# Performance work log

Measured on AMD Instinct MI355X. Metric: run time of the kernel, lower is better.

The kernel has to match this reference:

```python
import jax, jax.numpy as jnp
import numpy as np

N, E, IN, H, C, T = 50000, 800000, 128, 64, 64, 2
F1, FO1 = H, H // T   # conv1: per-tower in/out feats
F2, FO2 = H, C // T   # conv2
STD_EPS = 1e-5
BN_EPS = 1e-5


def setup_inputs() -> dict:
    key = jax.random.key(0)
    ks = jax.random.split(key, 12)
    rn = lambda k, s, sc=0.05: jax.random.normal(k, s, jnp.float32) * sc
    return {
        "x": jax.random.normal(ks[0], (N, IN), jnp.float32),
        "embed_W": rn(ks[1], (IN, H)),
        "embed_b": jnp.zeros((H,), jnp.float32),
        "pre_W1": rn(ks[2], (T, 2 * F1, F1)),
        "pre_b1": jnp.zeros((T, F1), jnp.float32),
        "post_W1": rn(ks[3], (T, 13 * F1, FO1)),
        "post_b1": jnp.zeros((T, FO1), jnp.float32),
        "lin_W1": rn(ks[4], (H, H)),
        "lin_b1": jnp.zeros((H,), jnp.float32),
        "bn_gamma": jnp.ones((H,), jnp.float32),
        "bn_beta": jnp.zeros((H,), jnp.float32),
        "pre_W2": rn(ks[5], (T, 2 * F2, F2)),
        "pre_b2": jnp.zeros((T, F2), jnp.float32),
        "post_W2": rn(ks[6], (T, 13 * F2, FO2)),
        "post_b2": jnp.zeros((T, FO2), jnp.float32),
        "lin_W2": rn(ks[7], (C, C)),
        "lin_b2": jnp.zeros((C,), jnp.float32),
        "src": jax.random.randint(ks[8], (E,), 0, N, jnp.int32),
        "dst": jax.random.randint(ks[9], (E,), 0, N, jnp.int32),
    }


def _pna_conv(h, src, dst, deg_raw, degc, avg_log, preW, preb, postW, postb, linW, linb):
    # h: [N, F] node feats; messages flow src -> dst, aggregated at dst.
    m = jnp.concatenate([h[dst], h[src]], axis=-1)            # [E, 2F]  (cat[x_i, x_j])
    m = jnp.einsum('ef,tfg->etg', m, preW) + preb[None]       # [E, T, F] per-tower pre-NN
    seg = lambda v: jax.ops.segment_sum(v, dst, num_segments=N)
    cnt = degc[:, None, None]                                 # clamped degree >= 1
    has = (deg_raw > 0)[:, None, None]
    mean = seg(m) / cnt                                       # [N, T, F]
    mean_sq = seg(m * m) / cnt
    mn = jnp.where(has, jax.ops.segment_min(m, dst, num_segments=N), 0.0)
    mx = jnp.where(has, jax.ops.segment_max(m, dst, num_segments=N), 0.0)
    std = jnp.sqrt(jax.nn.relu(mean_sq - mean * mean) + STD_EPS)
    agg = jnp.concatenate([mean, mn, mx, std], axis=-1)       # [N, T, 4F]
    ld = jnp.log(degc + 1.0)[:, None, None]
    out = jnp.concatenate([agg, agg * (ld / avg_log), agg * (avg_log / ld)], axis=-1)  # [N, T, 12F]
    F = h.shape[-1]
    out = jnp.concatenate([jnp.broadcast_to(h[:, None, :], (N, T, F)), out], axis=-1)  # [N, T, 13F]
    out = jnp.einsum('ntf,tfg->ntg', out, postW) + postb[None]  # [N, T, FO] per-tower post-NN
    return out.reshape(N, -1) @ linW + linb                    # final mixing Linear(out, out)


def reference(x, embed_W, embed_b, pre_W1, pre_b1, post_W1, post_b1, lin_W1, lin_b1,
              bn_gamma, bn_beta, pre_W2, pre_b2, post_W2, post_b2, lin_W2, lin_b2,
              src, dst):
    deg_raw = jax.ops.segment_sum(jnp.ones((E,), jnp.float32), dst, num_segments=N)
    degc = jnp.maximum(deg_raw, 1.0)
    avg_log = jnp.mean(jnp.log(deg_raw + 1.0))  # avg_deg['log'] from the graph's degrees
    h = x @ embed_W + embed_b
    h = _pna_conv(h, src, dst, deg_raw, degc, avg_log,
                  pre_W1, pre_b1, post_W1, post_b1, lin_W1, lin_b1)
    mu = jnp.mean(h, axis=0)
    var = jnp.mean((h - mu) ** 2, axis=0)
    h = bn_gamma * (h - mu) / jnp.sqrt(var + BN_EPS) + bn_beta
    h = jax.nn.relu(h)  # dropout is identity in eval mode
    return _pna_conv(h, src, dst, deg_raw, degc, avg_log,
                     pre_W2, pre_b2, post_W2, post_b2, lin_W2, lin_b2)
```

## Files before the change

kernel.cpp:

```cpp
#include <hip/hip_runtime.h>

#define N_NODES 50000
#define E_EDGES 800000
#define IN_F    128
#define H_F     64
#define STD_EPS 1e-5f
#define BN_EPS  1e-5f

#define HIST_BLK 3125
#define EMB_BLK  768
#define SCAN_BLK 49
#define TRANS_BLK 448

__global__ __launch_bounds__(256) void k_hist_embed(const int* __restrict__ dst,
                                                    int* __restrict__ deg,
                                                    const float* __restrict__ x,
                                                    const float* __restrict__ W,
                                                    const float* __restrict__ bias,
                                                    float* __restrict__ h) {
  __shared__ float sW[IN_F * 64];
  __shared__ float sx[IN_F * 36];
  if (blockIdx.x < HIST_BLK) {
    int e = blockIdx.x * 256 + threadIdx.x;
    atomicAdd(&deg[dst[e]], 1);
    return;
  }
  for (int i = threadIdx.x; i < IN_F * 64; i += 256) sW[i] = W[i];
  int f = threadIdx.x & 63, ng = threadIdx.x >> 6;
  float bj = bias[f];
  const int NGRP = (N_NODES + 31) / 32;
  for (int grp = blockIdx.x - HIST_BLK; grp < NGRP; grp += EMB_BLK) {
    int n0 = grp * 32;
    __syncthreads();
    for (int idx = threadIdx.x; idx < 32 * IN_F; idx += 256) {
      int nl = idx >> 7, k = idx & 127;
      int n = n0 + nl;
      sx[k * 36 + nl] = (n < N_NODES) ? x[(size_t)n * IN_F + k] : 0.f;
    }
    __syncthreads();
    float a[8] = {bj, bj, bj, bj, bj, bj, bj, bj};
    const float* xp = &sx[ng * 8];
#pragma unroll 4
    for (int k = 0; k < IN_F; k++) {
      float4 h0 = *(const float4*)&xp[k * 36];
      float4 h1 = *(const float4*)&xp[k * 36 + 4];
      float w = sW[k * 64 + f];
      a[0] = fmaf(h0.x, w, a[0]); a[1] = fmaf(h0.y, w, a[1]);
      a[2] = fmaf(h0.z, w, a[2]); a[3] = fmaf(h0.w, w, a[3]);
      a[4] = fmaf(h1.x, w, a[4]); a[5] = fmaf(h1.y, w, a[5]);
      a[6] = fmaf(h1.z, w, a[6]); a[7] = fmaf(h1.w, w, a[7]);
    }
#pragma unroll
    for (int j = 0; j < 8; j++) {
      int n = n0 + ng * 8 + j;
      if (n < N_NODES) h[(size_t)n * 64 + f] = a[j];
    }
  }
}

__global__ __launch_bounds__(256) void k_scanpart_trans(const int* __restrict__ deg,
                                                        int* __restrict__ partials,
                                                        float* __restrict__ scalars,
                                                        const float* __restrict__ pW1,
                                                        const float* __restrict__ pW2,
                                                        const float* __restrict__ lW1,
                                                        const float* __restrict__ lW2,
                                                        float* __restrict__ pWT,
                                                        float* __restrict__ lWT) {
  __shared__ int red[256];
  __shared__ float redf[256];
  if (blockIdx.x < SCAN_BLK) {
    int base = blockIdx.x * 1024;
    int s = 0; float ls = 0.f;
    for (int j = threadIdx.x; j < 1024; j += 256) {
      int i = base + j;
      if (i < N_NODES) { int d = deg[i]; s += d; ls += logf((float)d + 1.0f); }
    }
    red[threadIdx.x] = s; redf[threadIdx.x] = ls; __syncthreads();
    for (int st = 128; st > 0; st >>= 1) {
      if (threadIdx.x < st) {
        red[threadIdx.x] += red[threadIdx.x + st];
        redf[threadIdx.x] += redf[threadIdx.x + st];
      }
      __syncthreads();
    }
    if (threadIdx.x == 0) {
      partials[blockIdx.x] = red[0];
      atomicAdd(&scalars[0], redf[0]);
    }
    return;
  }
  int idx = (blockIdx.x - SCAN_BLK) * 256 + threadIdx.x;
  if (idx < 106496) {
    int layer = idx / 53248, r = idx % 53248;
    int t = r / 26624, r2 = r % 26624;
    int fb = r2 / 128, r3 = r2 % 128;
    int g = r3 / 4, j = r3 % 4;
    const float* srcp = layer ? pW2 : pW1;
    pWT[idx] = srcp[(size_t)t * 26624 + (fb * 4 + j) * 32 + g];
  } else if (idx < 114688) {
    int jj = idx - 106496;
    int layer = jj / 4096, r2 = jj % 4096;
    int c4 = r2 / 256, r3 = r2 % 256;
    int col = r3 / 4, j = r3 % 4;
    const float* srcl = layer ? lW2 : lW1;
    lWT[jj] = srcl[(c4 * 4 + j) * 64 + col];
  }
}

__global__ __launch_bounds__(256) void k_scan_final(const int* __restrict__ deg,
                                                    const int* __restrict__ partials,
                                                    int* __restrict__ row_ptr,
                                                    int* __restrict__ cursor,
                                                    float* __restrict__ scalars) {
  __shared__ int ts[256];
  __shared__ int sbase;
  if (threadIdx.x == 0) {
    int pre = 0;
    for (int b = 0; b < (int)blockIdx.x; b++) pre += partials[b];
    sbase = pre;
    if (blockIdx.x == 0) {
      scalars[1] = scalars[0] / (float)N_NODES;
      row_ptr[N_NODES] = E_EDGES;
    }
  }
  int base = blockIdx.x * 1024 + threadIdx.x * 4;
  int d[4]; int s = 0;
#pragma unroll
  for (int j = 0; j < 4; j++) {
    int i = base + j;
    d[j] = (i < N_NODES) ? deg[i] : 0;
    s += d[j];
  }
  ts[threadIdx.x] = s; __syncthreads();
  for (int off = 1; off < 256; off <<= 1) {
    int t = (threadIdx.x >= off) ? ts[threadIdx.x - off] : 0;
    __syncthreads();
    ts[threadIdx.x] += t;
    __syncthreads();
  }
  int excl = (threadIdx.x > 0) ? ts[threadIdx.x - 1] : 0;
  int run = sbase + excl;
#pragma unroll
  for (int j = 0; j < 4; j++) {
    int i = base + j;
    if (i < N_NODES) { row_ptr[i] = run; cursor[i] = run; run += d[j]; }
  }
}

__global__ __launch_bounds__(256) void k_scatter(const int* __restrict__ src,
                                                 const int* __restrict__ dst,
                                                 int* __restrict__ cursor,
                                                 int* __restrict__ csr_src) {
  int e = blockIdx.x * 256 + threadIdx.x;
  if (e < E_EDGES) {
    int d = dst[e];
    int p = atomicAdd(&cursor[d], 1);
    csr_src[p] = src[e];
  }
}

template <bool BN>
__global__ __launch_bounds__(256) void k_preab(const float* __restrict__ hin,
                                               const float* __restrict__ preW,
                                               const float* __restrict__ preb,
                                               const float* __restrict__ bnsum,
                                               const float* __restrict__ bnsumsq,
                                               const float* __restrict__ gamma,
                                               const float* __restrict__ beta,
                                               float* __restrict__ h2out,
                                               float* __restrict__ hA,
                                               float* __restrict__ hB) {
  __shared__ float sWp[64 * 128];
  __shared__ float sh[64 * 68];
  __shared__ float sbn[128];
  int t = blockIdx.x & 1;
  const float* Wsrc = preW + (size_t)t * 128 * 64;
  for (int i = threadIdx.x; i < 64 * 64; i += 256) {
    int k = i >> 6, f = i & 63;
    float wa = Wsrc[k * 64 + f];
    float wb = Wsrc[(64 + k) * 64 + f];
    *(float2*)&sWp[k * 128 + f * 2] = make_float2(wa, wb);
  }
  if (BN && threadIdx.x < 64) {
    int c = threadIdx.x;
    float mu = bnsum[c] * (1.f / N_NODES);
    float var = bnsumsq[c] * (1.f / N_NODES) - mu * mu;
    float sc = gamma[c] / sqrtf(var + BN_EPS);
    sbn[c] = sc;
    sbn[64 + c] = fmaf(-mu, sc, beta[c]);
  }
  int f = threadIdx.x & 63, ng = threadIdx.x >> 6;
  float pb = preb[t * 64 + f];
  int nblk2 = gridDim.x >> 1;
  const int NGRP = (N_NODES + 63) / 64;
  for (int grp = blockIdx.x >> 1; grp < NGRP; grp += nblk2) {
    int n0 = grp * 64;
    __syncthreads();
    for (int idx = threadIdx.x; idx < 64 * 64; idx += 256) {
      int nl = idx >> 6, k = idx & 63;
      int n = n0 + nl;
      float v = 0.f;
      if (n < N_NODES) {
        v = hin[(size_t)n * 64 + k];
        if (BN) {
          v = fmaxf(fmaf(v, sbn[k], sbn[64 + k]), 0.f);
          if (t == 0) h2out[(size_t)n * 64 + k] = v;
        }
      }
      sh[k * 68 + nl] = v;
    }
    __syncthreads();
    float a[16], b[16];
#pragma unroll
    for (int j = 0; j < 16; j++) { a[j] = pb; b[j] = 0.f; }
    const float* hp = &sh[ng * 16];
    const float* wp = &sWp[f * 2];
#pragma unroll 2
    for (int k = 0; k < 64; k++) {
      float4 h0 = *(const float4*)&hp[k * 68];
      float4 h1 = *(const float4*)&hp[k * 68 + 4];
      float4 h2 = *(const float4*)&hp[k * 68 + 8];
      float4 h3 = *(const float4*)&hp[k * 68 + 12];
      float2 w2 = *(const float2*)&wp[k * 128];
      a[0]  = fmaf(h0.x, w2.x, a[0]);  b[0]  = fmaf(h0.x, w2.y, b[0]);
      a[1]  = fmaf(h0.y, w2.x, a[1]);  b[1]  = fmaf(h0.y, w2.y, b[1]);
      a[2]  = fmaf(h0.z, w2.x, a[2]);  b[2]  = fmaf(h0.z, w2.y, b[2]);
      a[3]  = fmaf(h0.w, w2.x, a[3]);  b[3]  = fmaf(h0.w, w2.y, b[3]);
      a[4]  = fmaf(h1.x, w2.x, a[4]);  b[4]  = fmaf(h1.x, w2.y, b[4]);
      a[5]  = fmaf(h1.y, w2.x, a[5]);  b[5]  = fmaf(h1.y, w2.y, b[5]);
      a[6]  = fmaf(h1.z, w2.x, a[6]);  b[6]  = fmaf(h1.z, w2.y, b[6]);
      a[7]  = fmaf(h1.w, w2.x, a[7]);  b[7]  = fmaf(h1.w, w2.y, b[7]);
      a[8]  = fmaf(h2.x, w2.x, a[8]);  b[8]  = fmaf(h2.x, w2.y, b[8]);
      a[9]  = fmaf(h2.y, w2.x, a[9]);  b[9]  = fmaf(h2.y, w2.y, b[9]);
      a[10] = fmaf(h2.z, w2.x, a[10]); b[10] = fmaf(h2.z, w2.y, b[10]);
      a[11] = fmaf(h2.w, w2.x, a[11]); b[11] = fmaf(h2.w, w2.y, b[11]);
      a[12] = fmaf(h3.x, w2.x, a[12]); b[12] = fmaf(h3.x, w2.y, b[12]);
      a[13] = fmaf(h3.y, w2.x, a[13]); b[13] = fmaf(h3.y, w2.y, b[13]);
      a[14] = fmaf(h3.z, w2.x, a[14]); b[14] = fmaf(h3.z, w2.y, b[14]);
      a[15] = fmaf(h3.w, w2.x, a[15]); b[15] = fmaf(h3.w, w2.y, b[15]);
    }
    int tf = t * 64 + f;
#pragma unroll
    for (int j = 0; j < 16; j++) {
      int n = n0 + ng * 16 + j;
      if (n < N_NODES) {
        hA[(size_t)n * 128 + tf] = a[j];
        hB[(size_t)n * 128 + tf] = b[j];
      }
    }
  }
}

__global__ __launch_bounds__(256, 7) void k_conv(const float* __restrict__ hA,
                                                 const float* __restrict__ hB,
                                                 const float* __restrict__ hskip,
                                                 const int* __restrict__ row_ptr,
                                                 const int* __restrict__ csr_src,
                                                 const float* __restrict__ postWT,
                                                 const float* __restrict__ postb,
                                                 const float* __restrict__ linWT,
                                                 const float* __restrict__ linb,
                                                 const float* __restrict__ scalars,
                                                 float* __restrict__ out) {
  __shared__ float sm[2 * 5 * 8 * 64];
  __shared__ float sAB[16];
  int w = threadIdx.x >> 6, lane = threadIdx.x & 63;
  int n0 = blockIdx.x * 8;
  int t = lane >> 5, fb2 = (lane & 31) * 2;
  int off = t * 64 + fb2;
  float avg = scalars[1];

#pragma unroll 1
  for (int k = 0; k < 2; k++) {
    int nl = w * 2 + k;
    int n = n0 + nl;
    float2 a = *(const float2*)&hA[(size_t)n * 128 + off];
    int rp0 = __builtin_amdgcn_readfirstlane(row_ptr[n]);
    int rp1 = __builtin_amdgcn_readfirstlane(row_ptr[n + 1]);
    float sx0=0,sy0=0,qx0=0,qy0=0, sx1=0,sy1=0,qx1=0,qy1=0;
    float mnx0=INFINITY,mny0=INFINITY,mxx0=-INFINITY,mxy0=-INFINITY;
    float mnx1=INFINITY,mny1=INFINITY,mxx1=-INFINITY,mxy1=-INFINITY;
    int i = rp0;
    int end4 = rp0 + ((rp1 - rp0) & ~3);
    if (i < end4) {
      int s0 = csr_src[i], s1 = csr_src[i+1], s2 = csr_src[i+2], s3 = csr_src[i+3];
      while (true) {
        float2 v0 = *(const float2*)&hB[(size_t)s0 * 128 + off];
        float2 v1 = *(const float2*)&hB[(size_t)s1 * 128 + off];
        float2 v2 = *(const float2*)&hB[(size_t)s2 * 128 + off];
        float2 v3 = *(const float2*)&hB[(size_t)s3 * 128 + off];
        i += 4;
        bool more = (i < end4);
        if (more) { s0 = csr_src[i]; s1 = csr_src[i+1]; s2 = csr_src[i+2]; s3 = csr_src[i+3]; }
        float e0x = v0.x + a.x, e0y = v0.y + a.y;
        float e1x = v1.x + a.x, e1y = v1.y + a.y;
        float e2x = v2.x + a.x, e2y = v2.y + a.y;
        float e3x = v3.x + a.x, e3y = v3.y + a.y;
        sx0 += e0x; qx0 = fmaf(e0x,e0x,qx0); mnx0 = fminf(mnx0,e0x); mxx0 = fmaxf(mxx0,e0x);
        sy0 += e0y; qy0 = fmaf(e0y,e0y,qy0); mny0 = fminf(mny0,e0y); mxy0 = fmaxf(mxy0,e0y);
        sx1 += e1x; qx1 = fmaf(e1x,e1x,qx1); mnx1 = fminf(mnx1,e1x); mxx1 = fmaxf(mxx1,e1x);
        sy1 += e1y; qy1 = fmaf(e1y,e1y,qy1); mny1 = fminf(mny1,e1y); mxy1 = fmaxf(mxy1,e1y);
        sx0 += e2x; qx0 = fmaf(e2x,e2x,qx0); mnx0 = fminf(mnx0,e2x); mxx0 = fmaxf(mxx0,e2x);
        sy0 += e2y; qy0 = fmaf(e2y,e2y,qy0); mny0 = fminf(mny0,e2y); mxy0 = fmaxf(mxy0,e2y);
        sx1 += e3x; qx1 = fmaf(e3x,e3x,qx1); mnx1 = fminf(mnx1,e3x); mxx1 = fmaxf(mxx1,e3x);
        sy1 += e3y; qy1 = fmaf(e3y,e3y,qy1); mny1 = fminf(mny1,e3y); mxy1 = fmaxf(mxy1,e3y);
        if (!more) break;
      }
    }
    {
      int r = rp1 - i;
      if (r > 0) {
        int e1i = (r > 1) ? i + 1 : i;
        int e2i = (r > 2) ? i + 2 : i;
        int t0 = csr_src[i], t1 = csr_src[e1i], t2 = csr_src[e2i];
        float2 u0 = *(const float2*)&hB[(size_t)t0 * 128 + off];
        float2 u1 = *(const float2*)&hB[(size_t)t1 * 128 + off];
        float2 u2 = *(const float2*)&hB[(size_t)t2 * 128 + off];
        float ex = u0.x + a.x, ey = u0.y + a.y;
        sx0 += ex; qx0 = fmaf(ex,ex,qx0); mnx0 = fminf(mnx0,ex); mxx0 = fmaxf(mxx0,ex);
        sy0 += ey; qy0 = fmaf(ey,ey,qy0); mny0 = fminf(mny0,ey); mxy0 = fmaxf(mxy0,ey);
        if (r > 1) {
          ex = u1.x + a.x; ey = u1.y + a.y;
          sx1 += ex; qx1 = fmaf(ex,ex,qx1); mnx1 = fminf(mnx1,ex); mxx1 = fmaxf(mxx1,ex);
          sy1 += ey; qy1 = fmaf(ey,ey,qy1); mny1 = fminf(mny1,ey); mxy1 = fmaxf(mxy1,ey);
        }
        if (r > 2) {
          ex = u2.x + a.x; ey = u2.y + a.y;
          sx0 += ex; qx0 = fmaf(ex,ex,qx0); mnx0 = fminf(mnx0,ex); mxx0 = fmaxf(mxx0,ex);
          sy0 += ey; qy0 = fmaf(ey,ey,qy0); mny0 = fminf(mny0,ey); mxy0 = fmaxf(mxy0,ey);
        }
      }
    }
    int dg = rp1 - rp0;
    float cnt = (float)(dg > 0 ? dg : 1);
    float inv = 1.0f / cnt;
    float meanx = (sx0 + sx1) * inv, meany = (sy0 + sy1) * inv;
    float qx = qx0 + qx1, qy = qy0 + qy1;
    float sdx = sqrtf(fmaxf(qx * inv - meanx * meanx, 0.f) + STD_EPS);
    float sdy = sqrtf(fmaxf(qy * inv - meany * meany, 0.f) + STD_EPS);
    float mnx = fminf(mnx0, mnx1), mny = fminf(mny0, mny1);
    float mxx = fmaxf(mxx0, mxx1), mxy = fmaxf(mxy0, mxy1);
    if (dg == 0) { mnx = 0; mny = 0; mxx = 0; mxy = 0; }
    float ldv = logf(cnt + 1.f);
    float2 hsv = *(const float2*)&hskip[(size_t)n * 64 + fb2];
    float* bp = &sm[t * 2560 + nl * 64 + fb2];
    *(float2*)&bp[0]    = hsv;
    *(float2*)&bp[512]  = make_float2(meanx, meany);
    *(float2*)&bp[1024] = make_float2(mnx, mny);
    *(float2*)&bp[1536] = make_float2(mxx, mxy);
    *(float2*)&bp[2048] = make_float2(sdx, sdy);
    if (lane == 0) { sAB[nl] = ldv / avg; sAB[8 + nl] = avg / ldv; }
  }
  __syncthreads();

  float g1[8] = {0,0,0,0,0,0,0,0};
  float g2[8] = {0,0,0,0,0,0,0,0};
  float g3[8] = {0,0,0,0,0,0,0,0};
  {
    int g = lane & 31, hf0 = w * 16, fb0 = w * 4;
    const float4* pw4 = (const float4*)postWT + (size_t)t * 6656 + g;
    const float* vb = &sm[t * 2560 + hf0];
#pragma unroll
    for (int jj = 0; jj < 4; jj++) {
      float4 wv = pw4[(fb0 + jj) * 32];
#pragma unroll
      for (int nn = 0; nn < 8; nn++) {
        float4 v = *(const float4*)&vb[nn * 64 + jj * 4];
        g1[nn] = fmaf(v.w, wv.w, fmaf(v.z, wv.z, fmaf(v.y, wv.y, fmaf(v.x, wv.x, g1[nn]))));
      }
    }
#pragma unroll
    for (int fa = 0; fa < 4; fa++) {
      const float* vfa = &vb[(1 + fa) * 512];
#pragma unroll
      for (int jj = 0; jj < 4; jj++) {
        int fb = 16 + fa * 16 + fb0 + jj;
        float4 w1v = pw4[fb * 32];
        float4 w2v = pw4[(fb + 64) * 32];
        float4 w3v = pw4[(fb + 128) * 32];
#pragma unroll
        for (int nn = 0; nn < 8; nn++) {
          float4 v = *(const float4*)&vfa[nn * 64 + jj * 4];
          g1[nn] = fmaf(v.w, w1v.w, fmaf(v.z, w1v.z, fmaf(v.y, w1v.y, fmaf(v.x, w1v.x, g1[nn]))));
          g2[nn] = fmaf(v.w, w2v.w, fmaf(v.z, w2v.z, fmaf(v.y, w2v.y, fmaf(v.x, w2v.x, g2[nn]))));
          g3[nn] = fmaf(v.w, w3v.w, fmaf(v.z, w3v.z, fmaf(v.y, w3v.y, fmaf(v.x, w3v.x, g3[nn]))));
        }
      }
    }
  }
  float o8[8];
#pragma unroll
  for (int nn = 0; nn < 8; nn++)
    o8[nn] = fmaf(sAB[8 + nn], g3[nn], fmaf(sAB[nn], g2[nn], g1[nn]));
  __syncthreads();

  {
    int sw = (w + (lane >> 4)) & 3;
#pragma unroll
    for (int nn = 0; nn < 8; nn++)
      sm[((nn * 64 + lane) << 2) + sw] = o8[nn];
  }
  __syncthreads();

  {
#pragma unroll
    for (int r = 0; r < 2; r++) {
      int idx = r * 256 + (int)threadIdx.x;
      float4 p = *(const float4*)&sm[idx << 2];
      sm[2048 + idx] = p.x + p.y + p.z + p.w + postb[idx & 63];
    }
  }
  __syncthreads();

  {
    float acc0 = linb[lane], acc1 = acc0;
    const float4* lw4 = (const float4*)linWT + lane;
    const float* p0 = &sm[2048 + (w * 2) * 64];
    const float* p1 = p0 + 64;
#pragma unroll
    for (int c4 = 0; c4 < 16; c4++) {
      float4 lwv = lw4[c4 * 64];
      float4 pa = *(const float4*)&p0[c4 * 4];
      float4 pb2 = *(const float4*)&p1[c4 * 4];
      acc0 = fmaf(pa.w, lwv.w, fmaf(pa.z, lwv.z, fmaf(pa.y, lwv.y, fmaf(pa.x, lwv.x, acc0))));
      acc1 = fmaf(pb2.w, lwv.w, fmaf(pb2.z, lwv.z, fmaf(pb2.y, lwv.y, fmaf(pb2.x, lwv.x, acc1))));
    }
    size_t ob = (size_t)(n0 + w * 2) * 64 + lane;
    out[ob] = acc0;
    out[ob + 64] = acc1;
  }
}

__global__ __launch_bounds__(256) void k_bnstats(const float* __restrict__ y,
                                                 float* __restrict__ bnsum,
                                                 float* __restrict__ bnsumsq) {
  __shared__ float r1[256], r2[256];
  int c = threadIdx.x & 63, r = threadIdx.x >> 6;
  float s = 0, q = 0;
  for (int n = blockIdx.x * 4 + r; n < N_NODES; n += gridDim.x * 4) {
    float v = y[(size_t)n * 64 + c];
    s += v; q = fmaf(v, v, q);
  }
  r1[threadIdx.x] = s; r2[threadIdx.x] = q; __syncthreads();
  if (threadIdx.x < 64) {
    s = r1[threadIdx.x] + r1[threadIdx.x + 64] + r1[threadIdx.x + 128] + r1[threadIdx.x + 192];
    q = r2[threadIdx.x] + r2[threadIdx.x + 64] + r2[threadIdx.x + 128] + r2[threadIdx.x + 192];
    atomicAdd(&bnsum[threadIdx.x], s);
    atomicAdd(&bnsumsq[threadIdx.x], q);
  }
}

extern "C" void kernel_launch(void* const* d_in, const int* in_sizes, int n_in,
                              void* d_out, int out_size, void* d_ws, size_t ws_size,
                              hipStream_t stream) {
  const float* x      = (const float*)d_in[0];
  const float* embW   = (const float*)d_in[1];
  const float* embB   = (const float*)d_in[2];
  const float* preW1  = (const float*)d_in[3];
  const float* preb1  = (const float*)d_in[4];
  const float* postW1 = (const float*)d_in[5];
  const float* postb1 = (const float*)d_in[6];
  const float* linW1  = (const float*)d_in[7];
  const float* linb1  = (const float*)d_in[8];
  const float* gamma  = (const float*)d_in[9];
  const float* beta   = (const float*)d_in[10];
  const float* preW2  = (const float*)d_in[11];
  const float* preb2  = (const float*)d_in[12];
  const float* postW2 = (const float*)d_in[13];
  const float* postb2 = (const float*)d_in[14];
  const float* linW2  = (const float*)d_in[15];
  const float* linb2  = (const float*)d_in[16];
  const int*   src    = (const int*)d_in[17];
  const int*   dst    = (const int*)d_in[18];
  float* out = (float*)d_out;

  char* w = (char*)d_ws;
  size_t o = 0;
  int*   deg     = (int*)(w + o);   o += (size_t)N_NODES * 4;
  float* scalars = (float*)(w + o); o += 64;
  float* bnsum   = (float*)(w + o); o += 256;
  float* bnsumsq = (float*)(w + o); o += 256;
  size_t zero_len = o;
  o = (o + 255) & ~(size_t)255;
  int* partials = (int*)(w + o);  o += 256;
  int* row_ptr  = (int*)(w + o);  o += (size_t)(N_NODES + 1) * 4; o = (o + 255) & ~(size_t)255;
  int* cursor   = (int*)(w + o);  o += (size_t)N_NODES * 4;       o = (o + 255) & ~(size_t)255;
  int* csr      = (int*)(w + o);  o += (size_t)E_EDGES * 4;       o = (o + 255) & ~(size_t)255;
  float* postWT = (float*)(w + o); o += (size_t)2 * 53248 * 4;
  float* linWT  = (float*)(w + o); o += (size_t)2 * 4096 * 4;
  float* h1 = (float*)(w + o); o += (size_t)N_NODES * 64 * 4;
  float* y1 = (float*)(w + o); o += (size_t)N_NODES * 64 * 4;
  float* h2 = (float*)(w + o); o += (size_t)N_NODES * 64 * 4;
  float* hA = (float*)(w + o); o += (size_t)N_NODES * 128 * 4;
  float* hB = (float*)(w + o); o += (size_t)N_NODES * 128 * 4;

  hipMemsetAsync(w, 0, zero_len, stream);

  k_hist_embed<<<HIST_BLK + EMB_BLK, 256, 0, stream>>>(dst, deg, x, embW, embB, h1);
  k_scanpart_trans<<<SCAN_BLK + TRANS_BLK, 256, 0, stream>>>(
      deg, partials, scalars, postW1, postW2, linW1, linW2, postWT, linWT);
  k_scan_final<<<SCAN_BLK, 256, 0, stream>>>(deg, partials, row_ptr, cursor, scalars);
  k_scatter<<<(E_EDGES + 255) / 256, 256, 0, stream>>>(src, dst, cursor, csr);

  k_preab<false><<<768, 256, 0, stream>>>(h1, preW1, preb1, nullptr, nullptr,
                                          nullptr, nullptr, nullptr, hA, hB);
  k_conv<<<N_NODES / 8, 256, 0, stream>>>(hA, hB, h1, row_ptr, csr,
                                          postWT, postb1, linWT, linb1, scalars, y1);
  k_bnstats<<<256, 256, 0, stream>>>(y1, bnsum, bnsumsq);
  k_preab<true><<<768, 256, 0, stream>>>(y1, preW2, preb2, bnsum, bnsumsq,
                                         gamma, beta, h2, hA, hB);
  k_conv<<<N_NODES / 8, 256, 0, stream>>>(hA, hB, h2, row_ptr, csr,
                                          postWT + 53248, postb2, linWT + 4096,
                                          linb2, scalars, out);
}
```

Measured before the change: 540.5 us.

## Run per-tower post-NN GEMM on bf16x3 MFMA instead of FP32 FMAs

```diff
diff --git a/kernel.cpp b/kernel.cpp
--- a/kernel.cpp
+++ b/kernel.cpp
@@ -11,6 +11,23 @@
 #define EMB_BLK  768
 #define SCAN_BLK 49
 #define TRANS_BLK 448
+
+typedef __attribute__((ext_vector_type(8))) short bf16x8;
+typedef __attribute__((ext_vector_type(4))) float f32x4;
+
+__device__ __forceinline__ unsigned bf16_rne(float f) {
+  unsigned u = __float_as_uint(f);
+  return (u + 0x7fffu + ((u >> 16) & 1u)) >> 16;
+}
+__device__ __forceinline__ void bf16_split2(float x, float y, unsigned& hi, unsigned& lo) {
+  unsigned hx = bf16_rne(x), hy = bf16_rne(y);
+  float rx = x - __uint_as_float(hx << 16);
+  float ry = y - __uint_as_float(hy << 16);
+  hi = hx | (hy << 16);
+  lo = bf16_rne(rx) | (bf16_rne(ry) << 16);
+}
+
+#define MFMA(acc, a, b) acc = __builtin_amdgcn_mfma_f32_16x16x32_bf16(a, b, acc, 0, 0, 0)
 
 __global__ __launch_bounds__(256) void k_hist_embed(const int* __restrict__ dst,
                                                     int* __restrict__ deg,
@@ -65,7 +82,8 @@
                                                         const float* __restrict__ pW2,
                                                         const float* __restrict__ lW1,
                                                         const float* __restrict__ lW2,
-                                                        float* __restrict__ pWT,
+                                                        unsigned short* __restrict__ WBhi,
+                                                        unsigned short* __restrict__ WBlo,
                                                         float* __restrict__ lWT) {
   __shared__ int red[256];
   __shared__ float redf[256];
@@ -92,12 +110,15 @@
   }
   int idx = (blockIdx.x - SCAN_BLK) * 256 + threadIdx.x;
   if (idx < 106496) {
-    int layer = idx / 53248, r = idx % 53248;
-    int t = r / 26624, r2 = r % 26624;
-    int fb = r2 / 128, r3 = r2 % 128;
-    int g = r3 / 4, j = r3 % 4;
-    const float* srcp = layer ? pW2 : pW1;
-    pWT[idx] = srcp[(size_t)t * 26624 + (fb * 4 + j) * 32 + g];
+    int f = idx % 832;
+    int rest = idx / 832;
+    int col = rest & 31, tt = rest >> 5;
+    const float* srcp = (tt >= 2) ? pW2 : pW1;
+    float v = srcp[((size_t)(tt & 1) * 832 + f) * 32 + col];
+    unsigned hb = bf16_rne(v);
+    float rsd = v - __uint_as_float(hb << 16);
+    WBhi[idx] = (unsigned short)hb;
+    WBlo[idx] = (unsigned short)bf16_rne(rsd);
   } else if (idx < 114688) {
     int jj = idx - 106496;
     int layer = jj / 4096, r2 = jj % 4096;
@@ -252,18 +273,20 @@
   }
 }
 
-__global__ __launch_bounds__(256, 7) void k_conv(const float* __restrict__ hA,
+__global__ __launch_bounds__(256, 6) void k_conv(const float* __restrict__ hA,
                                                  const float* __restrict__ hB,
                                                  const float* __restrict__ hskip,
                                                  const int* __restrict__ row_ptr,
                                                  const int* __restrict__ csr_src,
-                                                 const float* __restrict__ postWT,
+                                                 const unsigned short* __restrict__ WBhi,
+                                                 const unsigned short* __restrict__ WBlo,
                                                  const float* __restrict__ postb,
                                                  const float* __restrict__ linWT,
                                                  const float* __restrict__ linb,
                                                  const float* __restrict__ scalars,
                                                  float* __restrict__ out) {
-  __shared__ float sm[2 * 5 * 8 * 64];
+  __shared__ unsigned sAhi[2688];
+  __shared__ unsigned sAlo[2688];
   __shared__ float sAB[16];
   int w = threadIdx.x >> 6, lane = threadIdx.x & 63;
   int n0 = blockIdx.x * 8;
@@ -344,91 +367,73 @@
     if (dg == 0) { mnx = 0; mny = 0; mxx = 0; mxy = 0; }
     float ldv = logf(cnt + 1.f);
     float2 hsv = *(const float2*)&hskip[(size_t)n * 64 + fb2];
-    float* bp = &sm[t * 2560 + nl * 64 + fb2];
-    *(float2*)&bp[0]    = hsv;
-    *(float2*)&bp[512]  = make_float2(meanx, meany);
-    *(float2*)&bp[1024] = make_float2(mnx, mny);
-    *(float2*)&bp[1536] = make_float2(mxx, mxy);
-    *(float2*)&bp[2048] = make_float2(sdx, sdy);
+    unsigned* ahp = &sAhi[(t * 8 + nl) * 168 + (fb2 >> 1)];
+    unsigned* alp = &sAlo[(t * 8 + nl) * 168 + (fb2 >> 1)];
+    unsigned hi, lo;
+    bf16_split2(hsv.x, hsv.y, hi, lo);   ahp[0]   = hi; alp[0]   = lo;
+    bf16_split2(meanx, meany, hi, lo);   ahp[32]  = hi; alp[32]  = lo;
+    bf16_split2(mnx, mny, hi, lo);       ahp[64]  = hi; alp[64]  = lo;
+    bf16_split2(mxx, mxy, hi, lo);       ahp[96]  = hi; alp[96]  = lo;
+    bf16_split2(sdx, sdy, hi, lo);       ahp[128] = hi; alp[128] = lo;
     if (lane == 0) { sAB[nl] = ldv / avg; sAB[8 + nl] = avg / ldv; }
   }
   __syncthreads();
 
-  float g1[8] = {0,0,0,0,0,0,0,0};
-  float g2[8] = {0,0,0,0,0,0,0,0};
-  float g3[8] = {0,0,0,0,0,0,0,0};
+  f32x4 acc1 = {0.f, 0.f, 0.f, 0.f};
+  f32x4 acc2 = {0.f, 0.f, 0.f, 0.f};
+  f32x4 acc3 = {0.f, 0.f, 0.f, 0.f};
+  int tw = w >> 1, ntile = w & 1;
+  int kq = lane >> 4;
   {
-    int g = lane & 31, hf0 = w * 16, fb0 = w * 4;
-    const float4* pw4 = (const float4*)postWT + (size_t)t * 6656 + g;
-    const float* vb = &sm[t * 2560 + hf0];
-#pragma unroll
-    for (int jj = 0; jj < 4; jj++) {
-      float4 wv = pw4[(fb0 + jj) * 32];
-#pragma unroll
-      for (int nn = 0; nn < 8; nn++) {
-        float4 v = *(const float4*)&vb[nn * 64 + jj * 4];
-        g1[nn] = fmaf(v.w, wv.w, fmaf(v.z, wv.z, fmaf(v.y, wv.y, fmaf(v.x, wv.x, g1[nn]))));
+    const bf16x8* Ah = (const bf16x8*)sAhi + (tw * 8 + (lane & 7)) * 42 + kq;
+    const bf16x8* Al = (const bf16x8*)sAlo + (tw * 8 + (lane & 7)) * 42 + kq;
+    int brow = (tw * 32 + ntile * 16 + (lane & 15)) * 104 + kq;
+    const bf16x8* Bh = (const bf16x8*)WBhi + brow;
+    const bf16x8* Bl = (const bf16x8*)WBlo + brow;
+#pragma unroll
+    for (int s = 0; s < 10; s++) {
+      bf16x8 ah = Ah[s * 4], al = Al[s * 4];
+      bf16x8 b1h = Bh[s * 4], b1l = Bl[s * 4];
+      MFMA(acc1, ah, b1h); MFMA(acc1, al, b1h); MFMA(acc1, ah, b1l);
+      if (s >= 2) {
+        bf16x8 b2h = Bh[40 + (s - 2) * 4], b2l = Bl[40 + (s - 2) * 4];
+        bf16x8 b3h = Bh[72 + (s - 2) * 4], b3l = Bl[72 + (s - 2) * 4];
+        MFMA(acc2, ah, b2h); MFMA(acc2, al, b2h); MFMA(acc2, ah, b2l);
+        MFMA(acc3, ah, b3h); MFMA(acc3, al, b3h); MFMA(acc3, ah, b3l);
       }
     }
-#pragma unroll
-    for (int fa = 0; fa < 4; fa++) {
-      const float* vfa = &vb[(1 + fa) * 512];
-#pragma unroll
-      for (int jj = 0; jj < 4; jj++) {
-        int fb = 16 + fa * 16 + fb0 + jj;
-        float4 w1v = pw4[fb * 32];
-        float4 w2v = pw4[(fb + 64) * 32];
-        float4 w3v = pw4[(fb + 128) * 32];
-#pragma unroll
-        for (int nn = 0; nn < 8; nn++) {
-          float4 v = *(const float4*)&vfa[nn * 64 + jj * 4];
-          g1[nn] = fmaf(v.w, w1v.w, fmaf(v.z, w1v.z, fmaf(v.y, w1v.y, fmaf(v.x, w1v.x, g1[nn]))));
-          g2[nn] = fmaf(v.w, w2v.w, fmaf(v.z, w2v.z, fmaf(v.y, w2v.y, fmaf(v.x, w2v.x, g2[nn]))));
-          g3[nn] = fmaf(v.w, w3v.w, fmaf(v.z, w3v.z, fmaf(v.y, w3v.y, fmaf(v.x, w3v.x, g3[nn]))));
-        }
-      }
-    }
-  }
-  float o8[8];
-#pragma unroll
-  for (int nn = 0; nn < 8; nn++)
-    o8[nn] = fmaf(sAB[8 + nn], g3[nn], fmaf(sAB[nn], g2[nn], g1[nn]));
+  }
   __syncthreads();
 
+  float* spo = (float*)sAhi;
+  if (lane < 32) {
+    int colg = tw * 32 + ntile * 16 + (lane & 15);
+    float pbv = postb[colg];
+    int rbase = kq * 4;
+#pragma unroll
+    for (int r = 0; r < 4; r++) {
+      int nr = rbase + r;
+      spo[nr * 64 + colg] = acc1[r] + sAB[nr] * acc2[r] + sAB[8 + nr] * acc3[r] + pbv;
+    }
+  }
+  __syncthreads();
+
   {
-    int sw = (w + (lane >> 4)) & 3;
-#pragma unroll
-    for (int nn = 0; nn < 8; nn++)
-      sm[((nn * 64 + lane) << 2) + sw] = o8[nn];
-  }
-  __syncthreads();
-
-  {
-#pragma unroll
-    for (int r = 0; r < 2; r++) {
-      int idx = r * 256 + (int)threadIdx.x;
-      float4 p = *(const float4*)&sm[idx << 2];
-      sm[2048 + idx] = p.x + p.y + p.z + p.w + postb[idx & 63];
-    }
-  }
-  __syncthreads();
-
-  {
-    float acc0 = linb[lane], acc1 = acc0;
+    float la0 = linb[lane], la1 = la0;
     const float4* lw4 = (const float4*)linWT + lane;
-    const float* p0 = &sm[2048 + (w * 2) * 64];
+    const float* p0 = &spo[(w * 2) * 64];
     const float* p1 = p0 + 64;
 #pragma unroll
     for (int c4 = 0; c4 < 16; c4++) {
       float4 lwv = lw4[c4 * 64];
       float4 pa = *(const float4*)&p0[c4 * 4];
       float4 pb2 = *(const float4*)&p1[c4 * 4];
-      acc0 = fmaf(pa.w, lwv.w, fmaf(pa.z, lwv.z, fmaf(pa.y, lwv.y, fmaf(pa.x, lwv.x, acc0))));
-      acc1 = fmaf(pb2.w, lwv.w, fmaf(pb2.z, lwv.z, fmaf(pb2.y, lwv.y, fmaf(pb2.x, lwv.x, acc1))));
+      la0 = fmaf(pa.w, lwv.w, fmaf(pa.z, lwv.z, fmaf(pa.y, lwv.y, fmaf(pa.x, lwv.x, la0))));
+      la1 = fmaf(pb2.w, lwv.w, fmaf(pb2.z, lwv.z, fmaf(pb2.y, lwv.y, fmaf(pb2.x, lwv.x, la1))));
     }
     size_t ob = (size_t)(n0 + w * 2) * 64 + lane;
-    out[ob] = acc0;
-    out[ob + 64] = acc1;
+    out[ob] = la0;
+    out[ob + 64] = la1;
   }
 }
 
@@ -487,7 +492,8 @@
   int* row_ptr  = (int*)(w + o);  o += (size_t)(N_NODES + 1) * 4; o = (o + 255) & ~(size_t)255;
   int* cursor   = (int*)(w + o);  o += (size_t)N_NODES * 4;       o = (o + 255) & ~(size_t)255;
   int* csr      = (int*)(w + o);  o += (size_t)E_EDGES * 4;       o = (o + 255) & ~(size_t)255;
-  float* postWT = (float*)(w + o); o += (size_t)2 * 53248 * 4;
+  unsigned short* WBhi = (unsigned short*)(w + o); o += (size_t)2 * 53248 * 2;
+  unsigned short* WBlo = (unsigned short*)(w + o); o += (size_t)2 * 53248 * 2;
   float* linWT  = (float*)(w + o); o += (size_t)2 * 4096 * 4;
   float* h1 = (float*)(w + o); o += (size_t)N_NODES * 64 * 4;
   float* y1 = (float*)(w + o); o += (size_t)N_NODES * 64 * 4;
@@ -499,18 +505,18 @@
 
   k_hist_embed<<<HIST_BLK + EMB_BLK, 256, 0, stream>>>(dst, deg, x, embW, embB, h1);
   k_scanpart_trans<<<SCAN_BLK + TRANS_BLK, 256, 0, stream>>>(
-      deg, partials, scalars, postW1, postW2, linW1, linW2, postWT, linWT);
+      deg, partials, scalars, postW1, postW2, linW1, linW2, WBhi, WBlo, linWT);
   k_scan_final<<<SCAN_BLK, 256, 0, stream>>>(deg, partials, row_ptr, cursor, scalars);
   k_scatter<<<(E_EDGES + 255) / 256, 256, 0, stream>>>(src, dst, cursor, csr);
 
   k_preab<false><<<768, 256, 0, stream>>>(h1, preW1, preb1, nullptr, nullptr,
                                           nullptr, nullptr, nullptr, hA, hB);
   k_conv<<<N_NODES / 8, 256, 0, stream>>>(hA, hB, h1, row_ptr, csr,
-                                          postWT, postb1, linWT, linb1, scalars, y1);
+                                          WBhi, WBlo, postb1, linWT, linb1, scalars, y1);
   k_bnstats<<<256, 256, 0, stream>>>(y1, bnsum, bnsumsq);
   k_preab<true><<<768, 256, 0, stream>>>(y1, preW2, preb2, bnsum, bnsumsq,
                                          gamma, beta, h2, hA, hB);
   k_conv<<<N_NODES / 8, 256, 0, stream>>>(hA, hB, h2, row_ptr, csr,
-                                          postWT + 53248, postb2, linWT + 4096,
-                                          linb2, scalars, out);
-}
+                                          WBhi + 53248, WBlo + 53248, postb2,
+                                          linWT + 4096, linb2, scalars, out);
+}
```

New measurement: 694.2 us. +28.4%, slower.
